# Kernel optimization log

Measured on AMD Instinct MI355X. Metric: run time of the kernel, lower is better.

The kernel has to match this reference:

```python
import jax, jax.numpy as jnp
import numpy as np

NUM_HEADS = 16
HEAD_DIM = 64
WINDOW = 512
D_MODEL = NUM_HEADS * HEAD_DIM
BATCH = 2
SEQ = 2048


def setup_inputs() -> dict:
    key = jax.random.key(0)
    k1, k2, k3 = jax.random.split(key, 3)
    x = jax.random.normal(k1, (BATCH, SEQ, D_MODEL), dtype=jnp.float32)
    # Dense layer params (lecun_normal-like scale for stability)
    qkv_kernel = jax.random.normal(k2, (D_MODEL, 3 * NUM_HEADS * HEAD_DIM), dtype=jnp.float32) / np.sqrt(D_MODEL)
    qkv_bias = jnp.zeros((3 * NUM_HEADS * HEAD_DIM,), dtype=jnp.float32)
    out_kernel = jax.random.normal(k3, (NUM_HEADS * HEAD_DIM, D_MODEL), dtype=jnp.float32) / np.sqrt(D_MODEL)
    out_bias = jnp.zeros((D_MODEL,), dtype=jnp.float32)
    return {"x": x, "qkv_kernel": qkv_kernel, "qkv_bias": qkv_bias,
            "out_kernel": out_kernel, "out_bias": out_bias}


def reference(x, qkv_kernel, qkv_bias, out_kernel, out_bias):
    b, s, d = x.shape
    qkv = x @ qkv_kernel + qkv_bias                       # (b, s, 3*H*hd)
    qkv = qkv.reshape(b, s, 3, NUM_HEADS, HEAD_DIM)
    q = qkv[:, :, 0].transpose(0, 2, 1, 3)                # (b, H, s, hd)
    k = qkv[:, :, 1].transpose(0, 2, 1, 3)
    v = qkv[:, :, 2].transpose(0, 2, 1, 3)
    scale = 1.0 / jnp.sqrt(jnp.float32(HEAD_DIM)).astype(x.dtype)
    scores = jnp.einsum('bhqd,bhkd->bhqk', q, k) * scale  # (b, H, s, s)
    rows = jnp.arange(s)[:, None]
    cols = jnp.arange(s)[None, :]
    window_mask = (rows - cols >= 0) & (rows - cols < WINDOW)
    scores = jnp.where(window_mask[None, None], scores, jnp.asarray(-1e9, scores.dtype))
    attn = jax.nn.softmax(scores, axis=-1)
    out = jnp.einsum('bhqk,bhkd->bhqd', attn, v)          # (b, H, s, hd)
    out = out.transpose(0, 2, 1, 3).reshape(b, s, -1)
    return out @ out_kernel + out_bias
```

## Files before the change

### kernel.cpp

```cpp
#include <hip/hip_runtime.h>
#include <cstdint>
#include <cstddef>

#define NUM_HEADS 16
#define HEAD_DIM  64
#define WINDOW    512
#define D_MODEL   1024
#define BATCH     2
#define SEQ       2048
#define MTOT      (BATCH*SEQ)
#define NQKV      (3*D_MODEL)

typedef short bf16x8 __attribute__((ext_vector_type(8)));
typedef float f32x4  __attribute__((ext_vector_type(4)));

__device__ __forceinline__ f32x4 mfma16(bf16x8 a, bf16x8 b, f32x4 c) {
  return __builtin_amdgcn_mfma_f32_16x16x32_bf16(a, b, c, 0, 0, 0);
}

__device__ __forceinline__ unsigned short f2bf(float f) {
  unsigned int u = __float_as_uint(f);
  u += 0x7fffu + ((u >> 16) & 1u);
  return (unsigned short)(u >> 16);
}
__device__ __forceinline__ float bf2f(unsigned short b) {
  return __uint_as_float(((unsigned int)b) << 16);
}

__device__ __forceinline__ void gld16(const unsigned short* g, unsigned short* l) {
  __builtin_amdgcn_global_load_lds(
      (const __attribute__((address_space(1))) unsigned int*)g,
      (__attribute__((address_space(3))) unsigned int*)l, 16, 0, 0);
}

__global__ __launch_bounds__(256) void prep_kernel(const float* __restrict__ x,
                                                   const float* __restrict__ qkv_w,
                                                   const float* __restrict__ out_w,
                                                   unsigned short* __restrict__ Xb,
                                                   unsigned short* __restrict__ Wq,
                                                   unsigned short* __restrict__ Wo) {
  __shared__ float tile[32][33];
  const int bid = blockIdx.x, t = threadIdx.x;
  if (bid < 4096) {
    int i = (bid * 256 + t) * 4;
    float4 v = *(const float4*)(x + i);
    ushort4 o;
    o.x = f2bf(v.x); o.y = f2bf(v.y); o.z = f2bf(v.z); o.w = f2bf(v.w);
    *(ushort4*)(Xb + i) = o;
    return;
  }
  const float* in; unsigned short* out; int R, C, bx, by;
  if (bid < 7168) { int b2 = bid - 4096; in = qkv_w; out = Wq; R = D_MODEL; C = NQKV; bx = b2 % 96; by = b2 / 96; }
  else            { int b2 = bid - 7168; in = out_w; out = Wo; R = D_MODEL; C = D_MODEL; bx = b2 & 31; by = b2 >> 5; }
  int tx = t & 31, ty = t >> 5;
  int c0 = bx * 32, r0 = by * 32;
#pragma unroll
  for (int i = 0; i < 32; i += 8)
    tile[ty + i][tx] = in[(size_t)(r0 + ty + i) * C + c0 + tx];
  __syncthreads();
#pragma unroll
  for (int i = 0; i < 32; i += 8)
    out[(size_t)(c0 + ty + i) * R + r0 + tx] = f2bf(tile[tx][ty + i]);
}

template<int TI, bool SWAP>
__device__ __forceinline__ void gemm_mainloop_db(const unsigned short* __restrict__ A,
                                                 const unsigned short* __restrict__ Bt,
                                                 int K, int m0, int n0,
                                                 unsigned short* sA0, unsigned short* sA1,
                                                 unsigned short* sB0, unsigned short* sB1,
                                                 f32x4 (&acc)[TI][4]) {
  const int t = threadIdx.x;
  const int lane = t & 63, wave = t >> 6;
  const int wm = wave >> 1, wn = wave & 1;
  const int lhi = lane >> 4, llo = lane & 15;
  f32x4 zero = {0.f, 0.f, 0.f, 0.f};
#pragma unroll
  for (int i = 0; i < TI; ++i)
#pragma unroll
    for (int j = 0; j < 4; ++j) acc[i][j] = zero;

  const int cswz = (((t & 3) ^ ((t >> 3) & 3)) << 3);
  const unsigned short* gA = A  + (size_t)(m0 + (t >> 2)) * K + cswz;
  const unsigned short* gB = Bt + (size_t)(n0 + (t >> 2)) * K + cswz;
  const size_t rowskip = (size_t)64 * K;
  const int ldsT = t * 8;
  const int rsw  = (lhi ^ ((llo >> 1) & 3)) * 8;
  const int aoff = (wm * (TI * 16) + llo) * 32 + rsw;
  const int boff = (wn * 64 + llo) * 32 + rsw;

  gld16(gA, sA0 + ldsT);
  if (TI == 4) gld16(gA + rowskip, sA0 + ldsT + 2048);
  gld16(gB, sB0 + ldsT);
  gld16(gB + rowskip, sB0 + ldsT + 2048);

  const int nIter = K >> 5;
  for (int it = 0; it < nIter; ++it) {
    __syncthreads();
    unsigned short* cA = (it & 1) ? sA1 : sA0;
    unsigned short* cB = (it & 1) ? sB1 : sB0;
    if (it + 1 < nIter) {
      unsigned short* nA = (it & 1) ? sA0 : sA1;
      unsigned short* nB = (it & 1) ? sB0 : sB1;
      gA += 32; gB += 32;
      gld16(gA, nA + ldsT);
      if (TI == 4) gld16(gA + rowskip, nA + ldsT + 2048);
      gld16(gB, nB + ldsT);
      gld16(gB + rowskip, nB + ldsT + 2048);
    }
    bf16x8 af[TI], bfr[4];
#pragma unroll
    for (int i = 0; i < TI; ++i) af[i]  = *(const bf16x8*)(cA + aoff + i * 512);
#pragma unroll
    for (int j = 0; j < 4; ++j)  bfr[j] = *(const bf16x8*)(cB + boff + j * 512);
#pragma unroll
    for (int i = 0; i < TI; ++i)
#pragma unroll
      for (int j = 0; j < 4; ++j)
        acc[i][j] = SWAP ? mfma16(bfr[j], af[i], acc[i][j])
                         : mfma16(af[i], bfr[j], acc[i][j]);
  }
}

__global__ __launch_bounds__(256) void qkv_gemm_kernel(const unsigned short* __restrict__ Xb,
                                                       const unsigned short* __restrict__ Wt,
                                                       const float* __restrict__ bias,
                                                       unsigned short* __restrict__ Qw,
                                                       unsigned short* __restrict__ Kw,
                                                       unsigned short* __restrict__ Vtw) {
  __shared__ __align__(16) unsigned short sA[2][128 * 32];
  __shared__ __align__(16) unsigned short sB[2][128 * 32];
  f32x4 acc[4][4];
  const int m0 = blockIdx.y * 128, n0 = blockIdx.x * 128;
  const int t = threadIdx.x, lane = t & 63, wave = t >> 6;
  const int wm = wave >> 1, wn = wave & 1, lhi = lane >> 4, llo = lane & 15;

  if (n0 < 2048) {
    gemm_mainloop_db<4, false>(Xb, Wt, D_MODEL, m0, n0, sA[0], sA[1], sB[0], sB[1], acc);
    const int c = n0 >> 10;
    unsigned short* __restrict__ Dst = (c == 0) ? Qw : Kw;
    const float qscale = (c == 0) ? 0.125f : 1.0f;
#pragma unroll
    for (int ti = 0; ti < 4; ++ti) {
#pragma unroll
      for (int tj = 0; tj < 4; ++tj) {
        int n = n0 + wn * 64 + tj * 16 + llo;
        float bv = bias[n];
        int h = (n >> 6) & 15, d = n & 63;
#pragma unroll
        for (int r = 0; r < 4; ++r) {
          int m = m0 + wm * 64 + ti * 16 + lhi * 4 + r;
          int b = m >> 11, s = m & 2047;
          int bh = b * 16 + h;
          Dst[((size_t)(bh * 2048 + s)) * 64 + d] = f2bf((acc[ti][tj][r] + bv) * qscale);
        }
      }
    }
  } else {
    gemm_mainloop_db<4, true>(Xb, Wt, D_MODEL, m0, n0, sA[0], sA[1], sB[0], sB[1], acc);
#pragma unroll
    for (int ti = 0; ti < 4; ++ti) {
      int m = m0 + wm * 64 + ti * 16 + llo;
      int b = m >> 11, s = m & 2047;
#pragma unroll
      for (int tj = 0; tj < 4; ++tj) {
        int nb = n0 + wn * 64 + tj * 16 + lhi * 4;
        float4 bv = *(const float4*)(bias + nb);
        int h = (nb >> 6) & 15, dbase = nb & 63;
        int bh = b * 16 + h;
        float bvr[4] = {bv.x, bv.y, bv.z, bv.w};
#pragma unroll
        for (int r = 0; r < 4; ++r)
          Vtw[(size_t)(bh * 64 + dbase + r) * 2048 + s] = f2bf(acc[ti][tj][r] + bvr[r]);
      }
    }
  }
}

__global__ __launch_bounds__(512) void attn_kernel(const unsigned short* __restrict__ Qw,
                                                   const unsigned short* __restrict__ Kw,
                                                   const unsigned short* __restrict__ Vtw,
                                                   unsigned short* __restrict__ AO) {
  __shared__ __align__(16) unsigned short sK[2][64 * 64];
  __shared__ __align__(16) unsigned short sV[2][64 * 64];
  __shared__ __align__(16) unsigned short sP[8][16 * 72];
  const int t = threadIdx.x, lane = t & 63, wave = t >> 6;
  const int lhi = lane >> 4, llo = lane & 15;
  const int bh = blockIdx.x;
  const int q0 = (15 - blockIdx.y) << 7;
  const unsigned short* Qb = Qw  + (size_t)bh * 2048 * 64;
  const unsigned short* Kb = Kw  + (size_t)bh * 2048 * 64;
  const unsigned short* Vb = Vtw + (size_t)bh * 64 * 2048;

  const int qw = q0 + wave * 16;
  const int qrow = qw + llo;
  bf16x8 qf0 = *(const bf16x8*)(Qb + (size_t)qrow * 64 + lhi * 8);
  bf16x8 qf1 = *(const bf16x8*)(Qb + (size_t)qrow * 64 + 32 + lhi * 8);

  const int srow = t >> 3;
  const int scol = ((t & 7) ^ (srow & 7)) * 8;
  const int cpos  = (lhi ^ (llo & 7)) * 8;
  const int cposx = cpos ^ 32;

  float m_i = -1e30f, l_i = 0.f;
  f32x4 o[4];
  f32x4 zero = {0.f, 0.f, 0.f, 0.f};
#pragma unroll
  for (int td = 0; td < 4; ++td) o[td] = zero;

  const int kt_lo = (q0 > 511) ? ((q0 - 511) >> 6) : 0;
  const int kt_hi = (q0 + 127) >> 6;

  {
    const int k0 = kt_lo << 6;
    unsigned short* dK = sK[kt_lo & 1];
    unsigned short* dV = sV[kt_lo & 1];
    gld16(Kb + (size_t)(k0 + srow) * 64 + scol, dK + t * 8);
    gld16(Vb + (size_t)srow * 2048 + k0 + scol, dV + t * 8);
  }

  for (int kt = kt_lo; kt <= kt_hi; ++kt) {
    __syncthreads();
    if (kt < kt_hi) {
      const int k0n = (kt + 1) << 6;
      unsigned short* dK = sK[(kt + 1) & 1];
      unsigned short* dV = sV[(kt + 1) & 1];
      gld16(Kb + (size_t)(k0n + srow) * 64 + scol, dK + t * 8);
      gld16(Vb + (size_t)srow * 2048 + k0n + scol, dV + t * 8);
    }
    const int k0 = kt << 6;
    if (k0 > qw + 15 || k0 + 63 < qw - (WINDOW - 1)) continue;

    const unsigned short* bK = sK[kt & 1];
    const unsigned short* bV = sV[kt & 1];

    f32x4 st[4];
#pragma unroll
    for (int tk = 0; tk < 4; ++tk) {
      const unsigned short* kr = bK + (tk * 16 + llo) * 64;
      bf16x8 kf0 = *(const bf16x8*)(kr + cpos);
      bf16x8 kf1 = *(const bf16x8*)(kr + cposx);
      f32x4 z = zero;
      z = mfma16(kf0, qf0, z);
      z = mfma16(kf1, qf1, z);
      st[tk] = z;
    }

    const int kb = k0 + lhi * 4;
    float mx = -1e30f;
#pragma unroll
    for (int tk = 0; tk < 4; ++tk)
#pragma unroll
      for (int r = 0; r < 4; ++r) {
        int key = kb + tk * 16 + r;
        bool ok = (key <= qrow) && (qrow - key < WINDOW);
        float s = ok ? st[tk][r] : -1e30f;
        st[tk][r] = s;
        mx = fmaxf(mx, s);
      }
    mx = fmaxf(mx, __shfl_xor(mx, 16));
    mx = fmaxf(mx, __shfl_xor(mx, 32));
    float mn = fmaxf(m_i, mx);
    float a  = __expf(m_i - mn);
    float rs = 0.f;
    unsigned short* pw = &sP[wave][llo * 72];
#pragma unroll
    for (int tk = 0; tk < 4; ++tk) {
      ushort4 pb;
      pb.x = f2bf(__expf(st[tk][0] - mn));
      pb.y = f2bf(__expf(st[tk][1] - mn));
      pb.z = f2bf(__expf(st[tk][2] - mn));
      pb.w = f2bf(__expf(st[tk][3] - mn));
      *(ushort4*)(pw + tk * 16 + lhi * 4) = pb;
      rs += bf2f(pb.x) + bf2f(pb.y) + bf2f(pb.z) + bf2f(pb.w);
    }
    rs += __shfl_xor(rs, 16);
    rs += __shfl_xor(rs, 32);
    l_i = l_i * a + rs;
    m_i = mn;

    float aR[4];
#pragma unroll
    for (int r = 0; r < 4; ++r) aR[r] = __shfl(a, lhi * 4 + r);
#pragma unroll
    for (int td = 0; td < 4; ++td)
#pragma unroll
      for (int r = 0; r < 4; ++r) o[td][r] *= aR[r];

    bf16x8 pf0 = *(const bf16x8*)(pw + lhi * 8);
    bf16x8 pf1 = *(const bf16x8*)(pw + 32 + lhi * 8);
#pragma unroll
    for (int td = 0; td < 4; ++td) {
      const unsigned short* vr = bV + (td * 16 + llo) * 64;
      bf16x8 vf0 = *(const bf16x8*)(vr + cpos);
      bf16x8 vf1 = *(const bf16x8*)(vr + cposx);
      o[td] = mfma16(pf0, vf0, o[td]);
      o[td] = mfma16(pf1, vf1, o[td]);
    }
  }

  float lR[4];
#pragma unroll
  for (int r = 0; r < 4; ++r) lR[r] = 1.f / __shfl(l_i, lhi * 4 + r);
  const int b = bh >> 4, h = bh & 15;
#pragma unroll
  for (int td = 0; td < 4; ++td)
#pragma unroll
    for (int r = 0; r < 4; ++r) {
      int qr = q0 + wave * 16 + lhi * 4 + r;
      AO[(size_t)(b * 2048 + qr) * 1024 + h * 64 + td * 16 + llo] = f2bf(o[td][r] * lR[r]);
    }
}

__global__ __launch_bounds__(256) void out_gemm_kernel(const unsigned short* __restrict__ AO,
                                                       const unsigned short* __restrict__ Wt,
                                                       const float* __restrict__ bias,
                                                       float* __restrict__ out) {
  __shared__ __align__(16) unsigned short sA[2][128 * 32];
  __shared__ __align__(16) unsigned short sB[2][128 * 32];
  f32x4 acc[4][4];
  const int m0 = blockIdx.y * 128, n0 = blockIdx.x * 128;
  gemm_mainloop_db<4, false>(AO, Wt, D_MODEL, m0, n0, sA[0], sA[1], sB[0], sB[1], acc);

  const int t = threadIdx.x, lane = t & 63, wave = t >> 6;
  const int wm = wave >> 1, wn = wave & 1, lhi = lane >> 4, llo = lane & 15;
#pragma unroll
  for (int ti = 0; ti < 4; ++ti)
#pragma unroll
    for (int tj = 0; tj < 4; ++tj) {
      int n = n0 + wn * 64 + tj * 16 + llo;
      float bv = bias[n];
#pragma unroll
      for (int r = 0; r < 4; ++r) {
        int m = m0 + wm * 64 + ti * 16 + lhi * 4 + r;
        out[(size_t)m * D_MODEL + n] = acc[ti][tj][r] + bv;
      }
    }
}

extern "C" void kernel_launch(void* const* d_in, const int* in_sizes, int n_in,
                              void* d_out, int out_size, void* d_ws, size_t ws_size,
                              hipStream_t stream) {
  const float* x      = (const float*)d_in[0];
  const float* qkv_w  = (const float*)d_in[1];
  const float* qkv_b  = (const float*)d_in[2];
  const float* out_w  = (const float*)d_in[3];
  const float* out_b  = (const float*)d_in[4];
  float* out = (float*)d_out;
  char* ws = (char*)d_ws;

  unsigned short* Xb  = (unsigned short*)(ws);
  unsigned short* Wq  = (unsigned short*)(ws + ((size_t)8  << 20));
  unsigned short* Wo  = (unsigned short*)(ws + ((size_t)14 << 20));
  unsigned short* Qw  = (unsigned short*)(ws + ((size_t)16 << 20));
  unsigned short* Kw  = (unsigned short*)(ws + ((size_t)24 << 20));
  unsigned short* Vtw = (unsigned short*)(ws + ((size_t)32 << 20));
  unsigned short* AO  = (unsigned short*)(ws + ((size_t)40 << 20));

  prep_kernel<<<8192, 256, 0, stream>>>(x, qkv_w, out_w, Xb, Wq, Wo);
  qkv_gemm_kernel<<<dim3(NQKV / 128, MTOT / 128), 256, 0, stream>>>(Xb, Wq, qkv_b, Qw, Kw, Vtw);
  attn_kernel<<<dim3(BATCH * NUM_HEADS, SEQ / 128), 512, 0, stream>>>(Qw, Kw, Vtw, AO);
  out_gemm_kernel<<<dim3(D_MODEL / 128, MTOT / 128), 256, 0, stream>>>(AO, Wo, out_b, out);
}
```

Baseline: 171.0 us.

## Switch GEMM and attention K/V loads to three-stage LDS pipeline with vmcnt waits

Replaces double-buffered LDS staging with a three-buffer ring in the QKV GEMM, output GEMM and attention kernels, issuing loads two iterations ahead. Uses explicit s_waitcnt vmcnt(N) plus s_barrier instead of __syncthreads, so only the oldest stage must have landed before compute starts. The GEMM K dimension becomes a template constant so the loop can be fully unrolled. This aims to hide global-to-LDS latency better, at the cost of more shared memory per block and hand-counted vmcnt values that must match the number of outstanding loads.

```diff
diff --git a/kernel.cpp b/kernel.cpp
--- a/kernel.cpp
+++ b/kernel.cpp
@@ -63,12 +63,11 @@
     out[(size_t)(c0 + ty + i) * R + r0 + tx] = f2bf(tile[tx][ty + i]);
 }
 
-template<int TI, bool SWAP>
-__device__ __forceinline__ void gemm_mainloop_db(const unsigned short* __restrict__ A,
+template<int TI, bool SWAP, int K>
+__device__ __forceinline__ void gemm_mainloop_p3(const unsigned short* __restrict__ A,
                                                  const unsigned short* __restrict__ Bt,
-                                                 int K, int m0, int n0,
-                                                 unsigned short* sA0, unsigned short* sA1,
-                                                 unsigned short* sB0, unsigned short* sB1,
+                                                 int m0, int n0,
+                                                 unsigned short* sA, unsigned short* sB,
                                                  f32x4 (&acc)[TI][4]) {
   const int t = threadIdx.x;
   const int lane = t & 63, wave = t >> 6;
@@ -88,26 +87,32 @@
   const int rsw  = (lhi ^ ((llo >> 1) & 3)) * 8;
   const int aoff = (wm * (TI * 16) + llo) * 32 + rsw;
   const int boff = (wn * 64 + llo) * 32 + rsw;
-
-  gld16(gA, sA0 + ldsT);
-  if (TI == 4) gld16(gA + rowskip, sA0 + ldsT + 2048);
-  gld16(gB, sB0 + ldsT);
-  gld16(gB + rowskip, sB0 + ldsT + 2048);
-
-  const int nIter = K >> 5;
+  constexpr int ABUF = TI * 1024;
+  constexpr int nIter = K / 32;
+
+  auto stage = [&](int it2) {
+    unsigned short* dA = sA + (it2 % 3) * ABUF;
+    unsigned short* dB = sB + (it2 % 3) * 4096;
+    const int kk = it2 * 32;
+    gld16(gA + kk, dA + ldsT);
+    if (TI == 4) gld16(gA + kk + rowskip, dA + ldsT + 2048);
+    gld16(gB + kk, dB + ldsT);
+    gld16(gB + kk + rowskip, dB + ldsT + 2048);
+  };
+
+  stage(0);
+  stage(1);
+#pragma unroll
   for (int it = 0; it < nIter; ++it) {
-    __syncthreads();
-    unsigned short* cA = (it & 1) ? sA1 : sA0;
-    unsigned short* cB = (it & 1) ? sB1 : sB0;
     if (it + 1 < nIter) {
-      unsigned short* nA = (it & 1) ? sA0 : sA1;
-      unsigned short* nB = (it & 1) ? sB0 : sB1;
-      gA += 32; gB += 32;
-      gld16(gA, nA + ldsT);
-      if (TI == 4) gld16(gA + rowskip, nA + ldsT + 2048);
-      gld16(gB, nB + ldsT);
-      gld16(gB + rowskip, nB + ldsT + 2048);
-    }
+      if (TI == 4) asm volatile("s_waitcnt vmcnt(4)\n\ts_barrier" ::: "memory");
+      else         asm volatile("s_waitcnt vmcnt(3)\n\ts_barrier" ::: "memory");
+    } else {
+      asm volatile("s_waitcnt vmcnt(0)\n\ts_barrier" ::: "memory");
+    }
+    if (it + 2 < nIter) stage(it + 2);
+    const unsigned short* cA = sA + (it % 3) * ABUF;
+    const unsigned short* cB = sB + (it % 3) * 4096;
     bf16x8 af[TI], bfr[4];
 #pragma unroll
     for (int i = 0; i < TI; ++i) af[i]  = *(const bf16x8*)(cA + aoff + i * 512);
@@ -128,15 +133,15 @@
                                                        unsigned short* __restrict__ Qw,
                                                        unsigned short* __restrict__ Kw,
                                                        unsigned short* __restrict__ Vtw) {
-  __shared__ __align__(16) unsigned short sA[2][128 * 32];
-  __shared__ __align__(16) unsigned short sB[2][128 * 32];
+  __shared__ __align__(16) unsigned short sA[3][128 * 32];
+  __shared__ __align__(16) unsigned short sB[3][128 * 32];
   f32x4 acc[4][4];
   const int m0 = blockIdx.y * 128, n0 = blockIdx.x * 128;
   const int t = threadIdx.x, lane = t & 63, wave = t >> 6;
   const int wm = wave >> 1, wn = wave & 1, lhi = lane >> 4, llo = lane & 15;
 
   if (n0 < 2048) {
-    gemm_mainloop_db<4, false>(Xb, Wt, D_MODEL, m0, n0, sA[0], sA[1], sB[0], sB[1], acc);
+    gemm_mainloop_p3<4, false, D_MODEL>(Xb, Wt, m0, n0, sA[0], sB[0], acc);
     const int c = n0 >> 10;
     unsigned short* __restrict__ Dst = (c == 0) ? Qw : Kw;
     const float qscale = (c == 0) ? 0.125f : 1.0f;
@@ -157,7 +162,7 @@
       }
     }
   } else {
-    gemm_mainloop_db<4, true>(Xb, Wt, D_MODEL, m0, n0, sA[0], sA[1], sB[0], sB[1], acc);
+    gemm_mainloop_p3<4, true, D_MODEL>(Xb, Wt, m0, n0, sA[0], sB[0], acc);
 #pragma unroll
     for (int ti = 0; ti < 4; ++ti) {
       int m = m0 + wm * 64 + ti * 16 + llo;
@@ -181,8 +186,8 @@
                                                    const unsigned short* __restrict__ Kw,
                                                    const unsigned short* __restrict__ Vtw,
                                                    unsigned short* __restrict__ AO) {
-  __shared__ __align__(16) unsigned short sK[2][64 * 64];
-  __shared__ __align__(16) unsigned short sV[2][64 * 64];
+  __shared__ __align__(16) unsigned short sK[3][64 * 64];
+  __shared__ __align__(16) unsigned short sV[3][64 * 64];
   __shared__ __align__(16) unsigned short sP[8][16 * 72];
   const int t = threadIdx.x, lane = t & 63, wave = t >> 6;
   const int lhi = lane >> 4, llo = lane & 15;
@@ -211,28 +216,26 @@
   const int kt_lo = (q0 > 511) ? ((q0 - 511) >> 6) : 0;
   const int kt_hi = (q0 + 127) >> 6;
 
-  {
-    const int k0 = kt_lo << 6;
-    unsigned short* dK = sK[kt_lo & 1];
-    unsigned short* dV = sV[kt_lo & 1];
+  auto stageKV = [&](int j) {
+    const int k0 = j << 6;
+    unsigned short* dK = sK[j % 3];
+    unsigned short* dV = sV[j % 3];
     gld16(Kb + (size_t)(k0 + srow) * 64 + scol, dK + t * 8);
     gld16(Vb + (size_t)srow * 2048 + k0 + scol, dV + t * 8);
-  }
+  };
+
+  stageKV(kt_lo);
+  stageKV(kt_lo + 1);
 
   for (int kt = kt_lo; kt <= kt_hi; ++kt) {
-    __syncthreads();
-    if (kt < kt_hi) {
-      const int k0n = (kt + 1) << 6;
-      unsigned short* dK = sK[(kt + 1) & 1];
-      unsigned short* dV = sV[(kt + 1) & 1];
-      gld16(Kb + (size_t)(k0n + srow) * 64 + scol, dK + t * 8);
-      gld16(Vb + (size_t)srow * 2048 + k0n + scol, dV + t * 8);
-    }
+    if (kt < kt_hi) asm volatile("s_waitcnt vmcnt(2)\n\ts_barrier" ::: "memory");
+    else            asm volatile("s_waitcnt vmcnt(0)\n\ts_barrier" ::: "memory");
+    if (kt + 2 <= kt_hi) stageKV(kt + 2);
     const int k0 = kt << 6;
     if (k0 > qw + 15 || k0 + 63 < qw - (WINDOW - 1)) continue;
 
-    const unsigned short* bK = sK[kt & 1];
-    const unsigned short* bV = sV[kt & 1];
+    const unsigned short* bK = sK[kt % 3];
+    const unsigned short* bV = sV[kt % 3];
 
     f32x4 st[4];
 #pragma unroll
@@ -316,11 +319,11 @@
                                                        const unsigned short* __restrict__ Wt,
                                                        const float* __restrict__ bias,
                                                        float* __restrict__ out) {
-  __shared__ __align__(16) unsigned short sA[2][128 * 32];
-  __shared__ __align__(16) unsigned short sB[2][128 * 32];
+  __shared__ __align__(16) unsigned short sA[3][128 * 32];
+  __shared__ __align__(16) unsigned short sB[3][128 * 32];
   f32x4 acc[4][4];
   const int m0 = blockIdx.y * 128, n0 = blockIdx.x * 128;
-  gemm_mainloop_db<4, false>(AO, Wt, D_MODEL, m0, n0, sA[0], sA[1], sB[0], sB[1], acc);
+  gemm_mainloop_p3<4, false, D_MODEL>(AO, Wt, m0, n0, sA[0], sB[0], acc);
 
   const int t = threadIdx.x, lane = t & 63, wave = t >> 6;
   const int wm = wave >> 1, wn = wave & 1, lhi = lane >> 4, llo = lane & 15;
```

New measurement: 169.8 us. Within noise of the previous version (-0.7%).
